# Kernel optimization log

Hardware: AMD Instinct MI355X
Metric: run time of the kernel (lower is better)

The kernel has to match this reference:

```python
import jax, jax.numpy as jnp
import numpy as np

K = 3  # unfold kernel size
K2 = K * K


def conv1x1_relu(x, w):
    # x: (B, C, H, W), w: (O, C)  -- BasicConv2d(channel, channel, 1, bias=False) + ReLU
    return jax.nn.relu(jnp.einsum('bchw,oc->bohw', x, w))


def unfold3x3(x, d=1):
    # torch nn.Unfold(kernel_size=3, padding=d, dilation=d): returns (B, C, 9, H, W)
    # with kernel index k = 3*i + j varying per channel block (channel-major, matching
    # the '(c k2)' split in the original rearrange).
    B, C, H, W = x.shape
    xp = jnp.pad(x, ((0, 0), (0, 0), (d, d), (d, d)))
    pats = [xp[:, :, i * d:i * d + H, j * d:j * d + W]
            for i in range(K) for j in range(K)]
    return jnp.stack(pats, axis=2)  # (B, C, 9, H, W)


def setup_inputs() -> dict:
    key = jax.random.key(0)
    k0, k1, k2, k3 = jax.random.split(key, 4)
    n, t, c, h, w = 2, 4, 64, 64, 96
    x = jax.random.normal(k0, (n, t, c, h, w), dtype=jnp.float32)
    # BasicConv2d inits conv weights with std=0.01
    w1 = jax.random.normal(k1, (c, c), dtype=jnp.float32) * 0.01
    w2 = jax.random.normal(k2, (c, c), dtype=jnp.float32) * 0.01
    w3 = jax.random.normal(k3, (c, c), dtype=jnp.float32) * 0.01
    return {'x': x, 'w1': w1, 'w2': w2, 'w3': w3}


def reference(x, w1, w2, w3):
    n, t, c, h, w = x.shape
    hw = h * w
    xf = x.reshape(n * t, c, h, w)

    x1 = unfold3x3(conv1x1_relu(xf, w1))  # (nt, c, 9, h, w)
    x2 = unfold3x3(conv1x1_relu(xf, w2))
    x3 = unfold3x3(conv1x1_relu(xf, w3))

    # x1: '(n t) (c k2) hw -> n hw t k2 c'
    x1 = x1.reshape(n, t, c, K2, hw).transpose(0, 4, 1, 3, 2)  # (n, hw, t, k2, c)
    x1_mean = jnp.mean(x1, axis=3)                              # (n, hw, t, c)
    x1_var = jnp.var(x1, axis=3, ddof=1)                        # unbiased
    x1f = x1.reshape(n, hw, t * K2, c)

    # x2: '(n t) (c k2) hw -> n hw c t k2'
    x2 = x2.reshape(n, t, c, K2, hw).transpose(0, 4, 2, 1, 3)   # (n, hw, c, t, k2)
    x2_mean = jnp.mean(x2, axis=4)                              # (n, hw, c, t)
    x2_var = jnp.var(x2, axis=4, ddof=1)
    x2f = x2.reshape(n, hw, c, t * K2)

    score1 = jax.nn.softmax(jnp.matmul(x1f, x2f), axis=-1)       # (n, hw, t*k2, t*k2)
    score2 = jax.nn.softmax(jnp.matmul(x1_var, x2_var), axis=-1) # (n, hw, t, t)
    score3 = jax.nn.softmax(jnp.matmul(x1_mean, x2_mean), axis=-1)

    # x3: '(n t) (c k2) hw -> n hw t (k2 c)'
    x3 = x3.reshape(n, t, c, K2, hw).transpose(0, 4, 1, 3, 2)   # (n, hw, t, k2, c)
    x3tk = x3.reshape(n, hw, t, K2 * c)
    x4 = jnp.matmul(score3, x3tk) + jnp.matmul(score2, x3tk)     # (n, hw, t, k2*c)
    x4 = x4.reshape(n, hw, t, K2, c)

    x3f = x3.reshape(n, hw, t * K2, c)
    x5 = jnp.matmul(score1, x3f).reshape(n, hw, t, K2, c)

    x6 = x5 + x4                                                 # (n, hw, t, k2, c)
    center = x6[:, :, :, K2 // 2, :][..., None]                  # (n, hw, t, c, 1)
    score4 = jax.nn.softmax(jnp.matmul(x6, center), axis=-2)     # (n, hw, t, k2, 1)
    out = jnp.sum(x6 * score4, axis=-2)                          # (n, hw, t, c)

    # 'n (h w) t c -> n t c h w'
    out = out.reshape(n, h, w, t, c).transpose(0, 3, 4, 1, 2)
    return out
```

## Files before the change

kernel.cpp:

```cpp
#include <hip/hip_runtime.h>

#define HW 6144
#define HH 64
#define WWID 96

typedef __attribute__((ext_vector_type(8))) _Float16 half8;
typedef __attribute__((ext_vector_type(2))) _Float16 half2v;
typedef __attribute__((ext_vector_type(8))) unsigned short ushort8;
typedef __attribute__((ext_vector_type(4))) float floatx4;
typedef __attribute__((ext_vector_type(4))) uint uint4v;

static __device__ __forceinline__ ushort f2h(float x) {
  _Float16 h = (_Float16)x;
  return __builtin_bit_cast(ushort, h);
}
static __device__ __forceinline__ float h2f(ushort b) {
  return (float)__builtin_bit_cast(_Float16, b);
}
static __device__ __forceinline__ uint pk2h(float a, float b) {
  return __builtin_bit_cast(uint, __builtin_amdgcn_cvt_pkrtz(a, b));
}
static __device__ __forceinline__ float hdot2(uint a, uint b, float c) {
#if __has_builtin(__builtin_amdgcn_fdot2)
  return __builtin_amdgcn_fdot2(__builtin_bit_cast(half2v, a),
                                __builtin_bit_cast(half2v, b), c, false);
#else
  c = fmaf(h2f((ushort)a), h2f((ushort)b), c);
  return fmaf(h2f((ushort)(a >> 16)), h2f((ushort)(b >> 16)), c);
#endif
}
static __device__ __forceinline__ half2v h2shfl16(half2v v) {
  return __builtin_bit_cast(half2v,
      (uint)__shfl_xor((int)__builtin_bit_cast(uint, v), 16));
}

__global__ __launch_bounds__(256) void conv_mfma_kernel(
    const float* __restrict__ X, const float* __restrict__ W1,
    const float* __restrict__ W2, const float* __restrict__ W3,
    ushort* __restrict__ Y1, ushort* __restrict__ Y2, ushort* __restrict__ Y3) {
  __shared__ __align__(16) ushort Xt[32 * 72];
  const int tid = threadIdx.x;
  const int wid = tid >> 6, lane = tid & 63;
  const int b = blockIdx.x / 192;
  const int p0 = (blockIdx.x % 192) * 32;

  if (blockIdx.x == 0 && tid < 32)
    ((uint*)(Y3 + (size_t)8 * HW * 64))[tid] = 0u;

#pragma unroll
  for (int it = 0; it < 2; ++it) {
    int idx = it * 256 + tid;
    int c = idx >> 3, pq = idx & 7;
    floatx4 v = *(const floatx4*)&X[((size_t)b * 64 + c) * HW + p0 + 4 * pq];
#pragma unroll
    for (int j = 0; j < 4; ++j) {
      int p = 4 * pq + j;
      Xt[p * 72 + (c ^ (p & 56))] = f2h(v[j]);
    }
  }
  __syncthreads();

  const int col = lane & 15, kg = lane >> 4;
  const int ph = wid & 1, mth = wid >> 1;
  const int p = ph * 16 + col;
  half8 b0 = *(const half8*)&Xt[p * 72 + ((kg * 8) ^ (p & 56))];
  half8 b1 = *(const half8*)&Xt[p * 72 + ((kg * 8 + 32) ^ (p & 56))];
  const size_t pixbase = ((size_t)b * HW + p0 + p) * 64;

  for (int s = 0; s < 3; ++s) {
    const float* Wf = (s == 0) ? W1 : (s == 1) ? W2 : W3;
    ushort* Y = (s == 0) ? Y1 : (s == 1) ? Y2 : Y3;
#pragma unroll
    for (int m = 0; m < 2; ++m) {
      int mt = mth * 2 + m;
      const float* wp = &Wf[(mt * 16 + col) * 64 + kg * 8];
      floatx4 w0 = *(const floatx4*)wp;
      floatx4 w1v = *(const floatx4*)(wp + 4);
      floatx4 w2v = *(const floatx4*)(wp + 32);
      floatx4 w3v = *(const floatx4*)(wp + 36);
      uint4v ua, ub;
      ua[0] = pk2h(w0[0], w0[1]);  ua[1] = pk2h(w0[2], w0[3]);
      ua[2] = pk2h(w1v[0], w1v[1]); ua[3] = pk2h(w1v[2], w1v[3]);
      ub[0] = pk2h(w2v[0], w2v[1]); ub[1] = pk2h(w2v[2], w2v[3]);
      ub[2] = pk2h(w3v[0], w3v[1]); ub[3] = pk2h(w3v[2], w3v[3]);
      half8 a0 = __builtin_bit_cast(half8, ua);
      half8 a1 = __builtin_bit_cast(half8, ub);
      floatx4 acc = {0.f, 0.f, 0.f, 0.f};
      acc = __builtin_amdgcn_mfma_f32_16x16x32_f16(a0, b0, acc, 0, 0, 0);
      acc = __builtin_amdgcn_mfma_f32_16x16x32_f16(a1, b1, acc, 0, 0, 0);
      uint2 u;
      u.x = pk2h(fmaxf(acc[0], 0.f), fmaxf(acc[1], 0.f));
      u.y = pk2h(fmaxf(acc[2], 0.f), fmaxf(acc[3], 0.f));
      *(uint2*)&Y[pixbase + mt * 16 + 4 * kg] = u;
    }
  }
}

__global__ __launch_bounds__(256, 6) void attn_kernel(
    const ushort* __restrict__ Y1, const ushort* __restrict__ Y2,
    const ushort* __restrict__ Y3, float* __restrict__ out) {
  __shared__ __align__(16) ushort XS[2 * 48 * 72];
  __shared__ __align__(16) ushort P1b[48 * 72];
  __shared__ uint mmv[2][128];
  __shared__ uint vvv[2][128];
  __shared__ int offv[64];
  __shared__ float SS2[16], SS3[16], Mm[16];
  __shared__ float L4[36];

  ushort* X1b = XS;
  ushort* X2b = XS + 48 * 72;
  float* X6f = (float*)XS;

  const int tid = threadIdx.x;
  const int wid = tid >> 6;
  const int lane = tid & 63;
  const int bid0 = blockIdx.x;
  const int bid = (bid0 & 7) * (12288 >> 3) + (bid0 >> 3);
  const int pix = bid % HW;
  const int nn = bid / HW;
  const int h = pix / WWID, w = pix - h * WWID;
  const int tb0 = nn * 4;

  {
    const int s = wid >> 1;
    const int t = (wid & 1) * 2 + (lane >> 5);
    const int kh = (lane >> 4) & 1;
    const int cq = lane & 15;
    const ushort* Ysrc = s ? Y2 : Y1;
    const int rowb = (tb0 + t) * HW;
    half2v s1a = {0, 0}, s1b = {0, 0}, s2a = {0, 0}, s2b = {0, 0};
#pragma unroll
    for (int i = 0; i < 5; ++i) {
      int k = 2 * i + kh;
      if (k < 9) {
        int k3 = (k * 11) >> 5;
        int hh = h + k3 - 1, ww = w + (k - 3 * k3) - 1;
        uint2 uv;
        uv.x = 0u; uv.y = 0u;
        if ((unsigned)hh < HH && (unsigned)ww < WWID)
          uv = *(const uint2*)&Ysrc[(rowb + hh * WWID + ww) * 64 + 4 * cq];
        *(uint2*)&XS[s * 3456 + (t * 9 + k) * 72 + 4 * cq] = uv;
        half2v va = __builtin_bit_cast(half2v, uv.x);
        half2v vb = __builtin_bit_cast(half2v, uv.y);
        s1a += va; s2a += va * va;
        s1b += vb; s2b += vb * vb;
      }
    }
    s1a += h2shfl16(s1a);
    s1b += h2shfl16(s1b);
    s2a += h2shfl16(s2a);
    s2b += h2shfl16(s2b);
    if (kh == 0) {
      float s1f[4] = {(float)s1a[0], (float)s1a[1], (float)s1b[0], (float)s1b[1]};
      float s2f[4] = {(float)s2a[0], (float)s2a[1], (float)s2b[0], (float)s2b[1]};
      float mf[4], vf[4];
#pragma unroll
      for (int j = 0; j < 4; ++j) {
        mf[j] = s1f[j] * (1.f / 9.f);
        vf[j] = (s2f[j] - s1f[j] * s1f[j] * (1.f / 9.f)) * 0.125f;
      }
      mmv[s][t * 32 + 2 * cq] = pk2h(mf[0], mf[1]);
      mmv[s][t * 32 + 2 * cq + 1] = pk2h(mf[2], mf[3]);
      vvv[s][t * 32 + 2 * cq] = pk2h(vf[0], vf[1]);
      vvv[s][t * 32 + 2 * cq + 1] = pk2h(vf[2], vf[3]);
    }
  }
  if (tid < 64) {
    int b = tid;
    int o = 2 * (8 * HW * 64);
    if (b < 36) {
      int t = (b * 57) >> 9;
      int k = b - 9 * t;
      int k3 = (k * 11) >> 5;
      int hh = h + k3 - 1, ww = w + (k - 3 * k3) - 1;
      if ((unsigned)hh < HH && (unsigned)ww < WWID)
        o = ((tb0 + t) * HW + hh * WWID + ww) * 128;
    }
    offv[b] = o;
  }
  for (int i = tid; i < 384; i += 256) {
    int r = i >> 3, u = i & 7;
    *(uint*)&P1b[r * 72 + 48 + 2 * u] = 0u;
  }
  for (int i = tid; i < 192; i += 256) {
    int r = i >> 4, cq = i & 15;
    uint2 z; z.x = 0u; z.y = 0u;
    *(uint2*)&X2b[(36 + r) * 72 + 4 * cq] = z;
  }
  __syncthreads();

  const int colL = lane & 15, kg = lane >> 4;
  const int c2 = (wid * 16 + colL) * 2;
  ushort8 xv0, xv1;
#pragma unroll
  for (int j = 0; j < 8; ++j) {
    xv0[j] = *(const ushort*)((const char*)Y3 + (offv[kg * 8 + j] + c2));
    xv1[j] = *(const ushort*)((const char*)Y3 + (offv[32 + kg * 8 + j] + c2));
  }

  if (wid < 3) {
    floatx4 ac0 = {0.f, 0.f, 0.f, 0.f}, ac1 = ac0, ac2 = ac0;
    int ar = (wid * 16 + colL) * 72 + (kg << 3);
    half8 a0 = *(const half8*)&X1b[ar];
    half8 a1 = *(const half8*)&X1b[ar + 32];
    int brb = colL * 72 + (kg << 3);
    ac0 = __builtin_amdgcn_mfma_f32_16x16x32_f16(a0, *(const half8*)&X2b[brb], ac0, 0, 0, 0);
    ac0 = __builtin_amdgcn_mfma_f32_16x16x32_f16(a1, *(const half8*)&X2b[brb + 32], ac0, 0, 0, 0);
    ac1 = __builtin_amdgcn_mfma_f32_16x16x32_f16(a0, *(const half8*)&X2b[brb + 16 * 72], ac1, 0, 0, 0);
    ac1 = __builtin_amdgcn_mfma_f32_16x16x32_f16(a1, *(const half8*)&X2b[brb + 16 * 72 + 32], ac1, 0, 0, 0);
    ac2 = __builtin_amdgcn_mfma_f32_16x16x32_f16(a0, *(const half8*)&X2b[brb + 32 * 72], ac2, 0, 0, 0);
    ac2 = __builtin_amdgcn_mfma_f32_16x16x32_f16(a1, *(const half8*)&X2b[brb + 32 * 72 + 32], ac2, 0, 0, 0);

    bool v2 = (colL < 4);
#pragma unroll
    for (int r = 0; r < 4; ++r) {
      float e0 = __expf(ac0[r]);
      float e1 = __expf(ac1[r]);
      float e2 = __expf(ac2[r]);
      float sm = e0 + e1 + (v2 ? e2 : 0.f);
#pragma unroll
      for (int d = 1; d < 16; d <<= 1) sm += __shfl_xor(sm, d);
      float rs = 1.f / sm;
      int ro = (wid * 16 + 4 * kg + r) * 72 + colL;
      P1b[ro] = f2h(e0 * rs);
      P1b[ro + 16] = f2h(e1 * rs);
      P1b[ro + 32] = f2h(e2 * rs);
    }
  } else {
    int pr = lane >> 2, q = lane & 3;
    int t1 = pr >> 2, t2 = pr & 3;
    float a3 = 0.f, a2 = 0.f;
#pragma unroll
    for (int j = 0; j < 8; ++j) {
      int cp = q * 8 + j;
      a3 = hdot2(mmv[0][t1 * 32 + cp], mmv[1][t2 * 32 + cp], a3);
      a2 = hdot2(vvv[0][t1 * 32 + cp], vvv[1][t2 * 32 + cp], a2);
    }
    a3 += __shfl_xor(a3, 1);
    a3 += __shfl_xor(a3, 2);
    a2 += __shfl_xor(a2, 1);
    a2 += __shfl_xor(a2, 2);
    if (q == 0) { SS3[pr] = a3; SS2[pr] = a2; }
    if (lane < 4) {
      float e3[4], e2v[4], s3 = 0.f, s2v = 0.f;
#pragma unroll
      for (int j = 0; j < 4; ++j) {
        e3[j] = __expf(SS3[lane * 4 + j]); s3 += e3[j];
        e2v[j] = __expf(SS2[lane * 4 + j]); s2v += e2v[j];
      }
      float r3 = 1.f / s3, r2 = 1.f / s2v;
#pragma unroll
      for (int j = 0; j < 4; ++j) Mm[lane * 4 + j] = fmaf(e3[j], r3, e2v[j] * r2);
    }
  }
  __syncthreads();

  if (tid < 144) {
    int a = tid >> 2, t2i = tid & 3;
    int ta = (a * 57) >> 9;
    int ka = a - 9 * ta;
    int off = a * 72 + t2i * 9 + ka;
    P1b[off] = f2h(h2f(P1b[off]) + Mm[ta * 4 + t2i]);
  }
  __syncthreads();

  {
    half8 xb0 = __builtin_bit_cast(half8, xv0);
    half8 xb1 = __builtin_bit_cast(half8, xv1);
    int c = wid * 16 + colL;
#pragma unroll
    for (int ti = 0; ti < 3; ++ti) {
      floatx4 acc = {0.f, 0.f, 0.f, 0.f};
      int ar = (ti * 16 + colL) * 72 + (kg << 3);
      acc = __builtin_amdgcn_mfma_f32_16x16x32_f16(*(const half8*)&P1b[ar], xb0, acc, 0, 0, 0);
      acc = __builtin_amdgcn_mfma_f32_16x16x32_f16(*(const half8*)&P1b[ar + 32], xb1, acc, 0, 0, 0);
      int r0 = ti * 16 + (kg << 2);
#pragma unroll
      for (int r = 0; r < 4; ++r) {
        int a = r0 + r;
        if (a < 36) X6f[a * 68 + c] = acc[r];
      }
    }
  }
  __syncthreads();

  if (tid < 144) {
    int a = tid >> 2, q = tid & 3;
    int ctr = ((a * 57) >> 9) * 9 + 4;
    const floatx4* rowA = (const floatx4*)&X6f[a * 68 + q * 16];
    const floatx4* rowC = (const floatx4*)&X6f[ctr * 68 + q * 16];
    float s = 0.f;
#pragma unroll
    for (int j = 0; j < 4; ++j) {
      floatx4 va = rowA[j], vc = rowC[j];
      s = fmaf(va[0], vc[0], s);
      s = fmaf(va[1], vc[1], s);
      s = fmaf(va[2], vc[2], s);
      s = fmaf(va[3], vc[3], s);
    }
    s += __shfl_xor(s, 1);
    s += __shfl_xor(s, 2);
    if (q == 0) L4[a] = s;
  }
  __syncthreads();

  {
    float den = 0.f, num = 0.f;
#pragma unroll
    for (int k = 0; k < 9; ++k) {
      float e = __expf(L4[wid * 9 + k]);
      den += e;
      num = fmaf(X6f[(wid * 9 + k) * 68 + lane], e, num);
    }
    out[((size_t)(tb0 + wid) * 64 + lane) * HW + pix] = num / den;
  }
}

extern "C" void kernel_launch(void* const* d_in, const int* in_sizes, int n_in,
                              void* d_out, int out_size, void* d_ws, size_t ws_size,
                              hipStream_t stream) {
  const float* x = (const float*)d_in[0];
  const float* w1 = (const float*)d_in[1];
  const float* w2 = (const float*)d_in[2];
  const float* w3 = (const float*)d_in[3];
  float* out = (float*)d_out;

  size_t ysz = (size_t)8 * HW * 64;
  ushort* Y1 = (ushort*)d_ws;
  ushort* Y2 = Y1 + ysz;
  ushort* Y3 = Y2 + ysz;

  conv_mfma_kernel<<<dim3(1536), dim3(256), 0, stream>>>(x, w1, w2, w3, Y1, Y2, Y3);
  attn_kernel<<<dim3(2 * HW), dim3(256), 0, stream>>>(Y1, Y2, Y3, out);
}
```

Measured before the change: 80.83 us.

## Shrink attention LDS footprint, use zero-sink loads, raise occupancy hint

Result: faster. 75.52 us (-6.6%).

```diff
diff --git a/kernel.cpp b/kernel.cpp
--- a/kernel.cpp
+++ b/kernel.cpp
@@ -9,6 +9,7 @@
 typedef __attribute__((ext_vector_type(8))) unsigned short ushort8;
 typedef __attribute__((ext_vector_type(4))) float floatx4;
 typedef __attribute__((ext_vector_type(4))) uint uint4v;
+typedef __attribute__((ext_vector_type(4))) int int4v;
 
 static __device__ __forceinline__ ushort f2h(float x) {
   _Float16 h = (_Float16)x;
@@ -44,8 +45,11 @@
   const int b = blockIdx.x / 192;
   const int p0 = (blockIdx.x % 192) * 32;
 
-  if (blockIdx.x == 0 && tid < 32)
-    ((uint*)(Y3 + (size_t)8 * HW * 64))[tid] = 0u;
+  if (blockIdx.x == 0 && tid < 96) {
+    int which = tid >> 5, i = tid & 31;
+    ushort* Ys = which == 0 ? Y1 : which == 1 ? Y2 : Y3;
+    ((uint*)(Ys + (size_t)8 * HW * 64))[i] = 0u;
+  }
 
 #pragma unroll
   for (int it = 0; it < 2; ++it) {
@@ -96,20 +100,19 @@
   }
 }
 
-__global__ __launch_bounds__(256, 6) void attn_kernel(
+__global__ __launch_bounds__(256, 7) void attn_kernel(
     const ushort* __restrict__ Y1, const ushort* __restrict__ Y2,
     const ushort* __restrict__ Y3, float* __restrict__ out) {
   __shared__ __align__(16) ushort XS[2 * 48 * 72];
   __shared__ __align__(16) ushort P1b[48 * 72];
-  __shared__ uint mmv[2][128];
-  __shared__ uint vvv[2][128];
-  __shared__ int offv[64];
-  __shared__ float SS2[16], SS3[16], Mm[16];
-  __shared__ float L4[36];
+  __shared__ __align__(16) uint mmv[2][128];
+  __shared__ __align__(16) uint vvv[2][128];
 
   ushort* X1b = XS;
   ushort* X2b = XS + 48 * 72;
   float* X6f = (float*)XS;
+  float* SSf = (float*)vvv;
+  float* L4f = (float*)mmv;
 
   const int tid = threadIdx.x;
   const int wid = tid >> 6;
@@ -120,6 +123,7 @@
   const int nn = bid / HW;
   const int h = pix / WWID, w = pix - h * WWID;
   const int tb0 = nn * 4;
+  const int SINKE = 8 * HW * 64;
 
   {
     const int s = wid >> 1;
@@ -127,18 +131,17 @@
     const int kh = (lane >> 4) & 1;
     const int cq = lane & 15;
     const ushort* Ysrc = s ? Y2 : Y1;
-    const int rowb = (tb0 + t) * HW;
+    const int base = (tb0 + t) * HW + pix;
     half2v s1a = {0, 0}, s1b = {0, 0}, s2a = {0, 0}, s2b = {0, 0};
 #pragma unroll
     for (int i = 0; i < 5; ++i) {
       int k = 2 * i + kh;
       if (k < 9) {
         int k3 = (k * 11) >> 5;
-        int hh = h + k3 - 1, ww = w + (k - 3 * k3) - 1;
-        uint2 uv;
-        uv.x = 0u; uv.y = 0u;
-        if ((unsigned)hh < HH && (unsigned)ww < WWID)
-          uv = *(const uint2*)&Ysrc[(rowb + hh * WWID + ww) * 64 + 4 * cq];
+        int dh = k3 - 1, dw = k - 3 * k3 - 1;
+        bool valid = ((unsigned)(h + dh) < HH) & ((unsigned)(w + dw) < WWID);
+        int off = valid ? (base + dh * WWID + dw) * 64 : SINKE;
+        uint2 uv = *(const uint2*)&Ysrc[off + 4 * cq];
         *(uint2*)&XS[s * 3456 + (t * 9 + k) * 72 + 4 * cq] = uv;
         half2v va = __builtin_bit_cast(half2v, uv.x);
         half2v vb = __builtin_bit_cast(half2v, uv.y);
@@ -167,7 +170,7 @@
   }
   if (tid < 64) {
     int b = tid;
-    int o = 2 * (8 * HW * 64);
+    int o = SINKE * 2;
     if (b < 36) {
       int t = (b * 57) >> 9;
       int k = b - 9 * t;
@@ -176,7 +179,7 @@
       if ((unsigned)hh < HH && (unsigned)ww < WWID)
         o = ((tb0 + t) * HW + hh * WWID + ww) * 128;
     }
-    offv[b] = o;
+    ((int*)&P1b[(b >> 2) * 72 + 64])[b & 3] = o;
   }
   for (int i = tid; i < 384; i += 256) {
     int r = i >> 3, u = i & 7;
@@ -190,12 +193,21 @@
   __syncthreads();
 
   const int colL = lane & 15, kg = lane >> 4;
-  const int c2 = (wid * 16 + colL) * 2;
   ushort8 xv0, xv1;
-#pragma unroll
-  for (int j = 0; j < 8; ++j) {
-    xv0[j] = *(const ushort*)((const char*)Y3 + (offv[kg * 8 + j] + c2));
-    xv1[j] = *(const ushort*)((const char*)Y3 + (offv[32 + kg * 8 + j] + c2));
+  {
+    const int c2 = (wid * 16 + colL) * 2;
+    const char* Y3b = (const char*)Y3;
+    int4v oa = *(const int4v*)&P1b[(kg * 2) * 72 + 64];
+    int4v ob = *(const int4v*)&P1b[(kg * 2 + 1) * 72 + 64];
+    int4v oc = *(const int4v*)&P1b[(kg * 2 + 8) * 72 + 64];
+    int4v od = *(const int4v*)&P1b[(kg * 2 + 9) * 72 + 64];
+#pragma unroll
+    for (int j = 0; j < 4; ++j) {
+      xv0[j] = *(const ushort*)(Y3b + (oa[j] + c2));
+      xv0[4 + j] = *(const ushort*)(Y3b + (ob[j] + c2));
+      xv1[j] = *(const ushort*)(Y3b + (oc[j] + c2));
+      xv1[4 + j] = *(const ushort*)(Y3b + (od[j] + c2));
+    }
   }
 
   if (wid < 3) {
@@ -240,17 +252,21 @@
     a3 += __shfl_xor(a3, 2);
     a2 += __shfl_xor(a2, 1);
     a2 += __shfl_xor(a2, 2);
-    if (q == 0) { SS3[pr] = a3; SS2[pr] = a2; }
+    if (q == 0) { SSf[pr] = a3; SSf[16 + pr] = a2; }
     if (lane < 4) {
+      floatx4 v3 = *(const floatx4*)&SSf[lane * 4];
+      floatx4 v2v = *(const floatx4*)&SSf[16 + lane * 4];
       float e3[4], e2v[4], s3 = 0.f, s2v = 0.f;
 #pragma unroll
       for (int j = 0; j < 4; ++j) {
-        e3[j] = __expf(SS3[lane * 4 + j]); s3 += e3[j];
-        e2v[j] = __expf(SS2[lane * 4 + j]); s2v += e2v[j];
+        e3[j] = __expf(v3[j]); s3 += e3[j];
+        e2v[j] = __expf(v2v[j]); s2v += e2v[j];
       }
       float r3 = 1.f / s3, r2 = 1.f / s2v;
-#pragma unroll
-      for (int j = 0; j < 4; ++j) Mm[lane * 4 + j] = fmaf(e3[j], r3, e2v[j] * r2);
+      floatx4 mm;
+#pragma unroll
+      for (int j = 0; j < 4; ++j) mm[j] = fmaf(e3[j], r3, e2v[j] * r2);
+      *(floatx4*)&SSf[32 + lane * 4] = mm;
     }
   }
   __syncthreads();
@@ -260,7 +276,7 @@
     int ta = (a * 57) >> 9;
     int ka = a - 9 * ta;
     int off = a * 72 + t2i * 9 + ka;
-    P1b[off] = f2h(h2f(P1b[off]) + Mm[ta * 4 + t2i]);
+    P1b[off] = f2h(h2f(P1b[off]) + SSf[32 + ta * 4 + t2i]);
   }
   __syncthreads();
 
@@ -300,7 +316,7 @@
     }
     s += __shfl_xor(s, 1);
     s += __shfl_xor(s, 2);
-    if (q == 0) L4[a] = s;
+    if (q == 0) L4f[a] = s;
   }
   __syncthreads();
 
@@ -308,7 +324,7 @@
     float den = 0.f, num = 0.f;
 #pragma unroll
     for (int k = 0; k < 9; ++k) {
-      float e = __expf(L4[wid * 9 + k]);
+      float e = __expf(L4f[wid * 9 + k]);
       den += e;
       num = fmaf(X6f[(wid * 9 + k) * 68 + lane], e, num);
     }
@@ -326,9 +342,10 @@
   float* out = (float*)d_out;
 
   size_t ysz = (size_t)8 * HW * 64;
+  size_t ypitch = ysz + 64;
   ushort* Y1 = (ushort*)d_ws;
-  ushort* Y2 = Y1 + ysz;
-  ushort* Y3 = Y2 + ysz;
+  ushort* Y2 = Y1 + ypitch;
+  ushort* Y3 = Y2 + ypitch;
 
   conv_mfma_kernel<<<dim3(1536), dim3(256), 0, stream>>>(x, w1, w2, w3, Y1, Y2, Y3);
   attn_kernel<<<dim3(2 * HW), dim3(256), 0, stream>>>(Y1, Y2, Y3, out);
```
